# Kernel optimization log

Hardware: AMD Instinct MI355X
Metric: run time of the kernel (lower is better)

## Reference

```python
import jax, jax.numpy as jnp
import numpy as np
from jax import lax

N_WIRES = 4
BN_EPS = 1e-5


def _conv2d_same(x, w, b):
    # x: [B,C,H,W], w: [O,I,3,3] -> 'SAME' padding == padding=1 for k=3
    y = lax.conv_general_dilated(x, w, window_strides=(1, 1), padding='SAME',
                                 dimension_numbers=('NCHW', 'OIHW', 'NCHW'))
    return y + b[None, :, None, None]


def _maxpool2(x):
    return lax.reduce_window(x, -jnp.inf, lax.max,
                             window_dimensions=(1, 1, 2, 2),
                             window_strides=(1, 1, 2, 2), padding='VALID')


def setup_inputs() -> dict:
    key = jax.random.key(0)
    ks = jax.random.split(key, 12)
    B = 8192
    x = jax.random.normal(ks[0], (B, 1, 28, 28), dtype=jnp.float32)
    params = jax.random.normal(ks[1], (B, N_WIRES), dtype=jnp.float32)  # per-sample circuit params
    conv1_w = jax.random.normal(ks[2], (8, 1, 3, 3), dtype=jnp.float32) * 0.1
    conv1_b = jnp.zeros((8,), jnp.float32)
    conv2_w = jax.random.normal(ks[3], (16, 8, 3, 3), dtype=jnp.float32) * 0.1
    conv2_b = jnp.zeros((16,), jnp.float32)
    qkv_w = jax.random.normal(ks[4], (3 * N_WIRES, 16 * 7 * 7), dtype=jnp.float32) * 0.03
    qkv_b = jnp.zeros((3 * N_WIRES,), jnp.float32)
    out_w = jax.random.normal(ks[5], (4, N_WIRES), dtype=jnp.float32) * 0.3
    out_b = jnp.zeros((4,), jnp.float32)
    bn_gamma = jnp.ones((4,), jnp.float32)
    bn_beta = jnp.zeros((4,), jnp.float32)
    return dict(x=x, params=params, conv1_w=conv1_w, conv1_b=conv1_b,
                conv2_w=conv2_w, conv2_b=conv2_b, qkv_w=qkv_w, qkv_b=qkv_b,
                out_w=out_w, out_b=out_b, bn_gamma=bn_gamma, bn_beta=bn_beta)


def reference(x, params, conv1_w, conv1_b, conv2_w, conv2_b,
              qkv_w, qkv_b, out_w, out_b, bn_gamma, bn_beta):
    # conv feature extractor: 28 -> 14 -> 7
    f = _maxpool2(jax.nn.relu(_conv2d_same(x, conv1_w, conv1_b)))
    f = _maxpool2(jax.nn.relu(_conv2d_same(f, conv2_w, conv2_b)))
    f_flat = f.reshape(f.shape[0], -1)                     # [B, 784]
    qkv = f_flat @ qkv_w.T + qkv_b                         # [B, 12]
    q, k, v = jnp.split(qkv, 3, axis=1)                    # each [B, 4]
    # Quantum circuit (4 qubits): RX(params[i]); RZ((q+k)[i]); CNOT chain; <Z_i>.
    # RZ is diagonal and commutes with every Z-string observable, so it drops out.
    # Heisenberg evolution through CNOT(0,1),CNOT(1,2),CNOT(2,3) gives
    # <Z_i> = prod_{j<=i} cos(params[j])  (vectorized over the batch).
    _ = q + k  # the circuit input; provably does not affect the expvals
    logits = jnp.cumprod(jnp.cos(params), axis=1)          # [B, 4]
    attn = jax.nn.softmax(logits, axis=1)
    out = attn * v                                         # [B, 4]
    out = out @ out_w.T + out_b                            # [B, 4]
    # BatchNorm1d in training mode: biased batch statistics
    mu = jnp.mean(out, axis=0)
    var = jnp.mean((out - mu) ** 2, axis=0)
    return (out - mu) / jnp.sqrt(var + BN_EPS) * bn_gamma + bn_beta
```

## Files before the change

### kernel.cpp

```cpp
#include <hip/hip_runtime.h>

#define BATCH 8192

__global__ __launch_bounds__(256) void prep(const float* __restrict__ c2w,
                                            float* __restrict__ w2r,
                                            float* __restrict__ partials) {
    int i = blockIdx.x * 256 + threadIdx.x;
    if (i < 1152) {
        int oc  = i & 15;
        int tic = i >> 4;
        int ic  = tic & 7;
        int tap = tic >> 3;
        w2r[i] = c2w[oc * 72 + ic * 9 + tap];
    }
    if (i < 2048) partials[i] = 0.f;
}

__global__ __launch_bounds__(256, 4) void fused_fwd(
    const float* __restrict__ x,
    const float* __restrict__ params,
    const float* __restrict__ c1w,
    const float* __restrict__ c1b,
    const float* __restrict__ c2b,
    const float* __restrict__ qkvw,
    const float* __restrict__ qkvb,
    const float* __restrict__ outw,
    const float* __restrict__ outb,
    const float* __restrict__ w2r,
    float* __restrict__ pre,
    float* __restrict__ partials)
{
    __shared__ __align__(16) float uA[3200];
    __shared__ __align__(16) float p1t[2304];
    __shared__ __align__(16) float p2[784];
    __shared__ float vred[4][4];

    const int tid = threadIdx.x;
    const int b = blockIdx.x;
    float* xs = uA;
    float* c2out = uA;

    for (int i = tid; i < 900; i += 256) {
        int h = i / 30, w = i - h * 30;
        float v = 0.f;
        if (h >= 1 && h <= 28 && w >= 1 && w <= 28)
            v = x[b * 784 + (h - 1) * 28 + (w - 1)];
        xs[i] = v;
    }
    for (int i = tid; i < 2304; i += 256) p1t[i] = 0.f;
    __syncthreads();

    {
        const int pos = tid < 196 ? tid : 195;
        const int ph = pos / 14, pw = pos - ph * 14;
        const float* base = &xs[(2 * ph) * 30 + 2 * pw];
        float in[4][4];
        #pragma unroll
        for (int r = 0; r < 4; ++r)
            #pragma unroll
            for (int c = 0; c < 4; ++c)
                in[r][c] = base[r * 30 + c];
        const int obase = ((ph + 1) * 16 + (pw + 1)) * 9;
        #pragma unroll
        for (int oc = 0; oc < 8; ++oc) {
            float m = 0.f;
            #pragma unroll
            for (int dh = 0; dh < 2; ++dh)
                #pragma unroll
                for (int dw = 0; dw < 2; ++dw) {
                    float a = c1b[oc];
                    #pragma unroll
                    for (int r = 0; r < 3; ++r)
                        #pragma unroll
                        for (int c = 0; c < 3; ++c)
                            a += in[dh + r][dw + c] * c1w[oc * 9 + r * 3 + c];
                    m = fmaxf(m, a);
                }
            if (tid < 196) p1t[obase + oc] = m;
        }
    }
    __syncthreads();

    {
        const int pos = tid < 196 ? tid : 195;
        const int h = pos / 14, w = pos - h * 14;
        const int pbase = (h * 16 + w) * 9;

        float a0  = c2b[0],  a1  = c2b[1],  a2  = c2b[2],  a3  = c2b[3];
        float a4  = c2b[4],  a5  = c2b[5],  a6  = c2b[6],  a7  = c2b[7];
        float a8  = c2b[8],  a9  = c2b[9],  a10 = c2b[10], a11 = c2b[11];
        float a12 = c2b[12], a13 = c2b[13], a14 = c2b[14], a15 = c2b[15];

        const float* wp = w2r;
        #pragma unroll 1
        for (int dh = 0; dh < 3; ++dh) {
            #pragma unroll 1
            for (int dw = 0; dw < 3; ++dw) {
                const int ibase = pbase + (dh * 16 + dw) * 9;
                #pragma unroll 1
                for (int ic = 0; ic < 8; ++ic) {
                    const float iv = p1t[ibase + ic];
                    const float4 w0 = *(const float4*)(wp + 0);
                    const float4 w1 = *(const float4*)(wp + 4);
                    const float4 w2 = *(const float4*)(wp + 8);
                    const float4 w3 = *(const float4*)(wp + 12);
                    a0  += iv * w0.x;  a1  += iv * w0.y;
                    a2  += iv * w0.z;  a3  += iv * w0.w;
                    a4  += iv * w1.x;  a5  += iv * w1.y;
                    a6  += iv * w1.z;  a7  += iv * w1.w;
                    a8  += iv * w2.x;  a9  += iv * w2.y;
                    a10 += iv * w2.z;  a11 += iv * w2.w;
                    a12 += iv * w3.x;  a13 += iv * w3.y;
                    a14 += iv * w3.z;  a15 += iv * w3.w;
                    wp += 16;
                }
            }
        }
        if (tid < 196) {
            c2out[0  * 200 + pos] = fmaxf(a0,  0.f);
            c2out[1  * 200 + pos] = fmaxf(a1,  0.f);
            c2out[2  * 200 + pos] = fmaxf(a2,  0.f);
            c2out[3  * 200 + pos] = fmaxf(a3,  0.f);
            c2out[4  * 200 + pos] = fmaxf(a4,  0.f);
            c2out[5  * 200 + pos] = fmaxf(a5,  0.f);
            c2out[6  * 200 + pos] = fmaxf(a6,  0.f);
            c2out[7  * 200 + pos] = fmaxf(a7,  0.f);
            c2out[8  * 200 + pos] = fmaxf(a8,  0.f);
            c2out[9  * 200 + pos] = fmaxf(a9,  0.f);
            c2out[10 * 200 + pos] = fmaxf(a10, 0.f);
            c2out[11 * 200 + pos] = fmaxf(a11, 0.f);
            c2out[12 * 200 + pos] = fmaxf(a12, 0.f);
            c2out[13 * 200 + pos] = fmaxf(a13, 0.f);
            c2out[14 * 200 + pos] = fmaxf(a14, 0.f);
            c2out[15 * 200 + pos] = fmaxf(a15, 0.f);
        }
    }
    __syncthreads();

    for (int it = tid; it < 784; it += 256) {
        int c = it / 49, r = it - c * 49;
        int ph = r / 7, pw = r - ph * 7;
        const float* pb = &c2out[c * 200 + (2 * ph) * 14 + 2 * pw];
        p2[it] = fmaxf(fmaxf(pb[0], pb[1]), fmaxf(pb[14], pb[15]));
    }
    __syncthreads();

    float v0 = 0.f, v1 = 0.f, v2 = 0.f, v3 = 0.f;
    if (tid < 196) {
        float4 f  = *(const float4*)&p2[tid * 4];
        float4 a0 = ((const float4*)&qkvw[8 * 784])[tid];
        float4 a1 = ((const float4*)&qkvw[9 * 784])[tid];
        float4 a2 = ((const float4*)&qkvw[10 * 784])[tid];
        float4 a3 = ((const float4*)&qkvw[11 * 784])[tid];
        v0 = f.x * a0.x + f.y * a0.y + f.z * a0.z + f.w * a0.w;
        v1 = f.x * a1.x + f.y * a1.y + f.z * a1.z + f.w * a1.w;
        v2 = f.x * a2.x + f.y * a2.y + f.z * a2.z + f.w * a2.w;
        v3 = f.x * a3.x + f.y * a3.y + f.z * a3.z + f.w * a3.w;
    }
    #pragma unroll
    for (int off = 32; off > 0; off >>= 1) {
        v0 += __shfl_xor(v0, off);
        v1 += __shfl_xor(v1, off);
        v2 += __shfl_xor(v2, off);
        v3 += __shfl_xor(v3, off);
    }
    if ((tid & 63) == 0) {
        const int wv = tid >> 6;
        vred[wv][0] = v0; vred[wv][1] = v1; vred[wv][2] = v2; vred[wv][3] = v3;
    }
    __syncthreads();

    if (tid < 4) {
        float vv[4];
        #pragma unroll
        for (int j = 0; j < 4; ++j)
            vv[j] = vred[0][j] + vred[1][j] + vred[2][j] + vred[3][j] + qkvb[8 + j];

        float lg[4];
        float run = 1.f;
        #pragma unroll
        for (int j = 0; j < 4; ++j) { run *= cosf(params[b * 4 + j]); lg[j] = run; }
        float mx = fmaxf(fmaxf(lg[0], lg[1]), fmaxf(lg[2], lg[3]));
        float e[4], s = 0.f;
        #pragma unroll
        for (int j = 0; j < 4; ++j) { e[j] = expf(lg[j] - mx); s += e[j]; }
        float inv = 1.f / s;

        float t = outb[tid];
        #pragma unroll
        for (int j = 0; j < 4; ++j) t += outw[tid * 4 + j] * (e[j] * inv * vv[j]);
        pre[b * 4 + tid] = t;
        atomicAdd(&partials[(b & 255) * 8 + tid], t);
        atomicAdd(&partials[(b & 255) * 8 + 4 + tid], t * t);
    }
}

__global__ __launch_bounds__(256) void bn_stats(
    const float* __restrict__ partials, float* __restrict__ stats)
{
    __shared__ float red[8][32];
    const int tid = threadIdx.x;
    const int val = tid & 7, grp = tid >> 3;
    float s = 0.f;
    for (int slot = grp; slot < 256; slot += 32) s += partials[slot * 8 + val];
    red[val][grp] = s;
    __syncthreads();
    if (tid < 8) {
        float t = 0.f;
        #pragma unroll
        for (int g = 0; g < 32; ++g) t += red[tid][g];
        red[tid][0] = t;
    }
    __syncthreads();
    if (tid < 4) {
        float mu  = red[tid][0] * (1.f / 8192.f);
        float var = red[tid + 4][0] * (1.f / 8192.f) - mu * mu;
        stats[tid]     = mu;
        stats[4 + tid] = rsqrtf(var + 1e-5f);
    }
}

__global__ __launch_bounds__(256) void bn_apply(
    const float* __restrict__ pre, const float* __restrict__ stats,
    const float* __restrict__ gamma, const float* __restrict__ beta,
    float* __restrict__ out)
{
    const int i = blockIdx.x * 256 + threadIdx.x;
    const int c = i & 3;
    out[i] = (pre[i] - stats[c]) * stats[4 + c] * gamma[c] + beta[c];
}

extern "C" void kernel_launch(void* const* d_in, const int* in_sizes, int n_in,
                              void* d_out, int out_size, void* d_ws, size_t ws_size,
                              hipStream_t stream) {
    const float* x      = (const float*)d_in[0];
    const float* params = (const float*)d_in[1];
    const float* c1w    = (const float*)d_in[2];
    const float* c1b    = (const float*)d_in[3];
    const float* c2w    = (const float*)d_in[4];
    const float* c2b    = (const float*)d_in[5];
    const float* qkvw   = (const float*)d_in[6];
    const float* qkvb   = (const float*)d_in[7];
    const float* outw   = (const float*)d_in[8];
    const float* outb   = (const float*)d_in[9];
    const float* gamma  = (const float*)d_in[10];
    const float* beta   = (const float*)d_in[11];

    float* ws       = (float*)d_ws;
    float* w2r      = ws;
    float* pre      = ws + 1152;
    float* partials = ws + 1152 + 32768;
    float* stats    = ws + 1152 + 32768 + 2048;

    prep<<<8, 256, 0, stream>>>(c2w, w2r, partials);
    fused_fwd<<<BATCH, 256, 0, stream>>>(x, params, c1w, c1b, c2b,
                                         qkvw, qkvb, outw, outb, w2r,
                                         pre, partials);
    bn_stats<<<1, 256, 0, stream>>>(partials, stats);
    bn_apply<<<32768 / 256, 256, 0, stream>>>(pre, stats, gamma, beta,
                                              (float*)d_out);
}
```

Measured before the change: 180.5 us.

## Fold weight prep into main kernel, drop atomics, fuse BN stats and apply

Removes the separate weight-reorder kernel by having each block load the reordered conv2 weights into LDS. It drops the per-sample atomic accumulation of BN partials and replaces the two BN kernels with a single kernel in which every block recomputes the batch sums from the pre-activations and then normalizes its own slice. This cuts launch count and atomic traffic. In exchange, each block does redundant reduction reads of the whole buffer and the main kernel does extra global-to-LDS weight loads.

```diff
diff --git a/kernel.cpp b/kernel.cpp
--- a/kernel.cpp
+++ b/kernel.cpp
@@ -1,44 +1,30 @@
 #include <hip/hip_runtime.h>
 
 #define BATCH 8192
-
-__global__ __launch_bounds__(256) void prep(const float* __restrict__ c2w,
-                                            float* __restrict__ w2r,
-                                            float* __restrict__ partials) {
-    int i = blockIdx.x * 256 + threadIdx.x;
-    if (i < 1152) {
-        int oc  = i & 15;
-        int tic = i >> 4;
-        int ic  = tic & 7;
-        int tap = tic >> 3;
-        w2r[i] = c2w[oc * 72 + ic * 9 + tap];
-    }
-    if (i < 2048) partials[i] = 0.f;
-}
 
 __global__ __launch_bounds__(256, 4) void fused_fwd(
     const float* __restrict__ x,
     const float* __restrict__ params,
     const float* __restrict__ c1w,
     const float* __restrict__ c1b,
+    const float* __restrict__ c2w,
     const float* __restrict__ c2b,
     const float* __restrict__ qkvw,
     const float* __restrict__ qkvb,
     const float* __restrict__ outw,
     const float* __restrict__ outb,
-    const float* __restrict__ w2r,
-    float* __restrict__ pre,
-    float* __restrict__ partials)
+    float* __restrict__ pre)
 {
-    __shared__ __align__(16) float uA[3200];
-    __shared__ __align__(16) float p1t[2304];
-    __shared__ __align__(16) float p2[784];
-    __shared__ float vred[4][4];
+    __shared__ __align__(16) float lds[6608];
+    float* xs    = lds;
+    float* c2out = lds;
+    float* p1t   = lds + 3136;
+    float* w2s   = lds + 5440;
+    float* p2    = lds + 5440;
+    float* vred  = lds + 6592;
 
     const int tid = threadIdx.x;
     const int b = blockIdx.x;
-    float* xs = uA;
-    float* c2out = uA;
 
     for (int i = tid; i < 900; i += 256) {
         int h = i / 30, w = i - h * 30;
@@ -48,6 +34,13 @@
         xs[i] = v;
     }
     for (int i = tid; i < 2304; i += 256) p1t[i] = 0.f;
+    for (int j = tid; j < 1152; j += 256) {
+        int oc  = j & 15;
+        int tic = j >> 4;
+        int ic  = tic & 7;
+        int tap = tic >> 3;
+        w2s[j] = c2w[oc * 72 + ic * 9 + tap];
+    }
     __syncthreads();
 
     {
@@ -91,7 +84,7 @@
         float a8  = c2b[8],  a9  = c2b[9],  a10 = c2b[10], a11 = c2b[11];
         float a12 = c2b[12], a13 = c2b[13], a14 = c2b[14], a15 = c2b[15];
 
-        const float* wp = w2r;
+        const float* wp = w2s;
         #pragma unroll 1
         for (int dh = 0; dh < 3; ++dh) {
             #pragma unroll 1
@@ -117,22 +110,22 @@
             }
         }
         if (tid < 196) {
-            c2out[0  * 200 + pos] = fmaxf(a0,  0.f);
-            c2out[1  * 200 + pos] = fmaxf(a1,  0.f);
-            c2out[2  * 200 + pos] = fmaxf(a2,  0.f);
-            c2out[3  * 200 + pos] = fmaxf(a3,  0.f);
-            c2out[4  * 200 + pos] = fmaxf(a4,  0.f);
-            c2out[5  * 200 + pos] = fmaxf(a5,  0.f);
-            c2out[6  * 200 + pos] = fmaxf(a6,  0.f);
-            c2out[7  * 200 + pos] = fmaxf(a7,  0.f);
-            c2out[8  * 200 + pos] = fmaxf(a8,  0.f);
-            c2out[9  * 200 + pos] = fmaxf(a9,  0.f);
-            c2out[10 * 200 + pos] = fmaxf(a10, 0.f);
-            c2out[11 * 200 + pos] = fmaxf(a11, 0.f);
-            c2out[12 * 200 + pos] = fmaxf(a12, 0.f);
-            c2out[13 * 200 + pos] = fmaxf(a13, 0.f);
-            c2out[14 * 200 + pos] = fmaxf(a14, 0.f);
-            c2out[15 * 200 + pos] = fmaxf(a15, 0.f);
+            c2out[0  * 196 + pos] = fmaxf(a0,  0.f);
+            c2out[1  * 196 + pos] = fmaxf(a1,  0.f);
+            c2out[2  * 196 + pos] = fmaxf(a2,  0.f);
+            c2out[3  * 196 + pos] = fmaxf(a3,  0.f);
+            c2out[4  * 196 + pos] = fmaxf(a4,  0.f);
+            c2out[5  * 196 + pos] = fmaxf(a5,  0.f);
+            c2out[6  * 196 + pos] = fmaxf(a6,  0.f);
+            c2out[7  * 196 + pos] = fmaxf(a7,  0.f);
+            c2out[8  * 196 + pos] = fmaxf(a8,  0.f);
+            c2out[9  * 196 + pos] = fmaxf(a9,  0.f);
+            c2out[10 * 196 + pos] = fmaxf(a10, 0.f);
+            c2out[11 * 196 + pos] = fmaxf(a11, 0.f);
+            c2out[12 * 196 + pos] = fmaxf(a12, 0.f);
+            c2out[13 * 196 + pos] = fmaxf(a13, 0.f);
+            c2out[14 * 196 + pos] = fmaxf(a14, 0.f);
+            c2out[15 * 196 + pos] = fmaxf(a15, 0.f);
         }
     }
     __syncthreads();
@@ -140,7 +133,7 @@
     for (int it = tid; it < 784; it += 256) {
         int c = it / 49, r = it - c * 49;
         int ph = r / 7, pw = r - ph * 7;
-        const float* pb = &c2out[c * 200 + (2 * ph) * 14 + 2 * pw];
+        const float* pb = &c2out[c * 196 + (2 * ph) * 14 + 2 * pw];
         p2[it] = fmaxf(fmaxf(pb[0], pb[1]), fmaxf(pb[14], pb[15]));
     }
     __syncthreads();
@@ -166,7 +159,8 @@
     }
     if ((tid & 63) == 0) {
         const int wv = tid >> 6;
-        vred[wv][0] = v0; vred[wv][1] = v1; vred[wv][2] = v2; vred[wv][3] = v3;
+        vred[wv * 4 + 0] = v0; vred[wv * 4 + 1] = v1;
+        vred[wv * 4 + 2] = v2; vred[wv * 4 + 3] = v3;
     }
     __syncthreads();
 
@@ -174,7 +168,8 @@
         float vv[4];
         #pragma unroll
         for (int j = 0; j < 4; ++j)
-            vv[j] = vred[0][j] + vred[1][j] + vred[2][j] + vred[3][j] + qkvb[8 + j];
+            vv[j] = vred[0 + j] + vred[4 + j] + vred[8 + j] + vred[12 + j]
+                  + qkvb[8 + j];
 
         float lg[4];
         float run = 1.f;
@@ -190,44 +185,60 @@
         #pragma unroll
         for (int j = 0; j < 4; ++j) t += outw[tid * 4 + j] * (e[j] * inv * vv[j]);
         pre[b * 4 + tid] = t;
-        atomicAdd(&partials[(b & 255) * 8 + tid], t);
-        atomicAdd(&partials[(b & 255) * 8 + 4 + tid], t * t);
     }
 }
 
-__global__ __launch_bounds__(256) void bn_stats(
-    const float* __restrict__ partials, float* __restrict__ stats)
+__global__ __launch_bounds__(256) void bn_final(
+    const float* __restrict__ pre, const float* __restrict__ gamma,
+    const float* __restrict__ beta, float* __restrict__ out)
 {
-    __shared__ float red[8][32];
+    __shared__ float red[4][8];
     const int tid = threadIdx.x;
-    const int val = tid & 7, grp = tid >> 3;
-    float s = 0.f;
-    for (int slot = grp; slot < 256; slot += 32) s += partials[slot * 8 + val];
-    red[val][grp] = s;
-    __syncthreads();
-    if (tid < 8) {
-        float t = 0.f;
-        #pragma unroll
-        for (int g = 0; g < 32; ++g) t += red[tid][g];
-        red[tid][0] = t;
-    }
-    __syncthreads();
-    if (tid < 4) {
-        float mu  = red[tid][0] * (1.f / 8192.f);
-        float var = red[tid + 4][0] * (1.f / 8192.f) - mu * mu;
-        stats[tid]     = mu;
-        stats[4 + tid] = rsqrtf(var + 1e-5f);
-    }
-}
-
-__global__ __launch_bounds__(256) void bn_apply(
-    const float* __restrict__ pre, const float* __restrict__ stats,
-    const float* __restrict__ gamma, const float* __restrict__ beta,
-    float* __restrict__ out)
-{
-    const int i = blockIdx.x * 256 + threadIdx.x;
-    const int c = i & 3;
-    out[i] = (pre[i] - stats[c]) * stats[4 + c] * gamma[c] + beta[c];
+    const float4* pre4 = (const float4*)pre;
+
+    float4 s = make_float4(0.f, 0.f, 0.f, 0.f);
+    float4 q = make_float4(0.f, 0.f, 0.f, 0.f);
+    for (int i = tid; i < 8192; i += 256) {
+        float4 v = pre4[i];
+        s.x += v.x; s.y += v.y; s.z += v.z; s.w += v.w;
+        q.x += v.x * v.x; q.y += v.y * v.y; q.z += v.z * v.z; q.w += v.w * v.w;
+    }
+    #pragma unroll
+    for (int off = 32; off > 0; off >>= 1) {
+        s.x += __shfl_xor(s.x, off); s.y += __shfl_xor(s.y, off);
+        s.z += __shfl_xor(s.z, off); s.w += __shfl_xor(s.w, off);
+        q.x += __shfl_xor(q.x, off); q.y += __shfl_xor(q.y, off);
+        q.z += __shfl_xor(q.z, off); q.w += __shfl_xor(q.w, off);
+    }
+    if ((tid & 63) == 0) {
+        const int wv = tid >> 6;
+        red[wv][0] = s.x; red[wv][1] = s.y; red[wv][2] = s.z; red[wv][3] = s.w;
+        red[wv][4] = q.x; red[wv][5] = q.y; red[wv][6] = q.z; red[wv][7] = q.w;
+    }
+    __syncthreads();
+
+    float mu[4], inv[4];
+    #pragma unroll
+    for (int c = 0; c < 4; ++c) {
+        float ts = red[0][c] + red[1][c] + red[2][c] + red[3][c];
+        float tq = red[0][4 + c] + red[1][4 + c] + red[2][4 + c] + red[3][4 + c];
+        float m = ts * (1.f / 8192.f);
+        mu[c] = m;
+        inv[c] = rsqrtf(tq * (1.f / 8192.f) - m * m + 1e-5f);
+    }
+
+    if (tid < 64) {
+        const int i = blockIdx.x * 64 + tid;
+        float4 v = pre4[i];
+        float4 g = *(const float4*)gamma;
+        float4 be = *(const float4*)beta;
+        float4 o;
+        o.x = (v.x - mu[0]) * inv[0] * g.x + be.x;
+        o.y = (v.y - mu[1]) * inv[1] * g.y + be.y;
+        o.z = (v.z - mu[2]) * inv[2] * g.z + be.z;
+        o.w = (v.w - mu[3]) * inv[3] * g.w + be.w;
+        ((float4*)out)[i] = o;
+    }
 }
 
 extern "C" void kernel_launch(void* const* d_in, const int* in_sizes, int n_in,
@@ -246,17 +257,9 @@
     const float* gamma  = (const float*)d_in[10];
     const float* beta   = (const float*)d_in[11];
 
-    float* ws       = (float*)d_ws;
-    float* w2r      = ws;
-    float* pre      = ws + 1152;
-    float* partials = ws + 1152 + 32768;
-    float* stats    = ws + 1152 + 32768 + 2048;
-
-    prep<<<8, 256, 0, stream>>>(c2w, w2r, partials);
-    fused_fwd<<<BATCH, 256, 0, stream>>>(x, params, c1w, c1b, c2b,
-                                         qkvw, qkvb, outw, outb, w2r,
-                                         pre, partials);
-    bn_stats<<<1, 256, 0, stream>>>(partials, stats);
-    bn_apply<<<32768 / 256, 256, 0, stream>>>(pre, stats, gamma, beta,
-                                              (float*)d_out);
+    float* pre = (float*)d_ws;
+
+    fused_fwd<<<BATCH, 256, 0, stream>>>(x, params, c1w, c1b, c2w, c2b,
+                                         qkvw, qkvb, outw, outb, pre);
+    bn_final<<<128, 256, 0, stream>>>(pre, gamma, beta, (float*)d_out);
 }
```

New measurement: 204.3 us. +13.2%, slower.
